# Kernel optimization log

Measured on AMD Instinct MI355X. Metric: run time of the kernel, lower is better.

Reference implementation:

```python
import jax, jax.numpy as jnp
import numpy as np

N = 8192
TEMP = 0.5
EPS = 1e-12


def _normalize(z):
    # F.normalize(z, p=2, dim=1): x / max(||x||, eps)
    n = jnp.sqrt(jnp.sum(z * z, axis=1, keepdims=True))
    return z / jnp.maximum(n, EPS)


def _gcn(edge_index, edge_weight, x, w, b):
    # torch.sparse.mm(adj, x @ w): out[row] += adj[row, col] * support[col]
    support = x @ w
    msg = support[edge_index[1]] * edge_weight[:, None]
    return jax.ops.segment_sum(msg, edge_index[0], num_segments=N) + b


def _encoder(edge_index, edge_weight, feat, w_l1a, b_l1a, w_l1b, b_l1b, w_g1, b_g1, w_g2, b_g2):
    x = jax.nn.relu(feat @ w_l1a + b_l1a) @ w_l1b + b_l1b  # [N, 32]
    h = jax.nn.relu(_gcn(edge_index, edge_weight, x, w_g1, b_g1))  # [N, hid]
    return _gcn(edge_index, edge_weight, h, w_g2, b_g2)  # [N, act_fn]


def _proj(h, w_fc1, b_fc1, w_fc2, b_fc2):
    return jax.nn.elu(h @ w_fc1 + b_fc1) @ w_fc2 + b_fc2


def _loss(z1, z2):
    z1n = _normalize(z1)
    z2n = _normalize(z2)
    refl = jnp.exp((z1n @ z1n.T) / TEMP)      # [N, N]
    between = jnp.exp((z1n @ z2n.T) / TEMP)   # [N, N]
    denom = refl.sum(1) + between.sum(1) - jnp.diagonal(refl)
    return -jnp.log(jnp.diagonal(between) / denom)


def setup_inputs() -> dict:
    key = jax.random.key(0)
    ks = jax.random.split(key, 20)
    E = 262144
    in_dim, hid_dim, act_fn, out_dim = 512, 256, 128, 64

    def kaiming(k, shape):
        fan_in = shape[0]
        bound = np.sqrt(6.0 / fan_in)
        return jax.random.uniform(k, shape, jnp.float32, -bound, bound)

    return {
        "feat1": jax.random.normal(ks[0], (N, in_dim), jnp.float32),
        "feat2": jax.random.normal(ks[1], (N, in_dim), jnp.float32),
        "edge_index1": jax.random.randint(ks[2], (2, E), 0, N, jnp.int32),
        "edge_weight1": jax.random.uniform(ks[3], (E,), jnp.float32),
        "edge_index2": jax.random.randint(ks[4], (2, E), 0, N, jnp.int32),
        "edge_weight2": jax.random.uniform(ks[5], (E,), jnp.float32),
        "w_l1a": kaiming(ks[6], (in_dim, 64)),
        "b_l1a": jnp.zeros((64,), jnp.float32),
        "w_l1b": kaiming(ks[7], (64, 32)),
        "b_l1b": jnp.zeros((32,), jnp.float32),
        "w_g1": kaiming(ks[8], (32, hid_dim)),
        "b_g1": jnp.zeros((hid_dim,), jnp.float32),
        "w_g2": kaiming(ks[9], (hid_dim, act_fn)),
        "b_g2": jnp.zeros((act_fn,), jnp.float32),
        "w_fc1": kaiming(ks[10], (act_fn, out_dim)),
        "b_fc1": jnp.zeros((out_dim,), jnp.float32),
        "w_fc2": kaiming(ks[11], (out_dim, act_fn)),
        "b_fc2": jnp.zeros((act_fn,), jnp.float32),
    }


def reference(feat1, feat2, edge_index1, edge_weight1, edge_index2, edge_weight2,
              w_l1a, b_l1a, w_l1b, b_l1b, w_g1, b_g1, w_g2, b_g2,
              w_fc1, b_fc1, w_fc2, b_fc2):
    h1 = _encoder(edge_index1, edge_weight1, feat1, w_l1a, b_l1a, w_l1b, b_l1b, w_g1, b_g1, w_g2, b_g2)
    h2 = _encoder(edge_index2, edge_weight2, feat2, w_l1a, b_l1a, w_l1b, b_l1b, w_g1, b_g1, w_g2, b_g2)
    z1 = _proj(h1, w_fc1, b_fc1, w_fc2, b_fc2)
    z2 = _proj(h2, w_fc1, b_fc1, w_fc2, b_fc2)
    l1 = _loss(z1, z2)
    l2 = _loss(z2, z1)
    return ((l1 + l2) * 0.5).mean()
```

## Files before the change

kernel.cpp:

```cpp
#include <hip/hip_runtime.h>
#include <hip/hip_bf16.h>
#include <math.h>


#define NROWS 8192
#define MROWS 16384
#define NEDGE 262144
#define ECAP 128

typedef __attribute__((ext_vector_type(8))) short bf16x8;
typedef __attribute__((ext_vector_type(4))) float f32x4;
typedef __attribute__((ext_vector_type(2))) float f32x2;
typedef __attribute__((ext_vector_type(8))) int i32x8;
typedef long long i64;

__device__ __forceinline__ short f2bf(float f){
  union { float f; unsigned u; } cv; cv.f = f;
  unsigned u = cv.u;
  unsigned r = (u + 0x7fffu + ((u >> 16) & 1u)) >> 16;
  return (short)r;
}
__device__ __forceinline__ f32x4 mfma16(bf16x8 a, bf16x8 b, f32x4 c){
  return __builtin_amdgcn_mfma_f32_16x16x32_bf16(a, b, c, 0, 0, 0);
}
__device__ __forceinline__ float fexp2(float x){
#if __has_builtin(__builtin_amdgcn_exp2f)
  return __builtin_amdgcn_exp2f(x);
#else
  return exp2f(x);
#endif
}

template<int CTRL>
__device__ __forceinline__ float dpp_add(float v){
  int s = __builtin_amdgcn_update_dpp(0, __builtin_bit_cast(int, v),
                                      CTRL, 0xf, 0xf, true);
  return v + __builtin_bit_cast(float, s);
}
__device__ __forceinline__ float red16(float v){
  v = dpp_add<0x101>(v);
  v = dpp_add<0x102>(v);
  v = dpp_add<0x104>(v);
  v = dpp_add<0x108>(v);
  return v;
}

__device__ unsigned char f2e4m3_sw(float f){
  float a = fabsf(f);
  unsigned s = (__float_as_uint(f)>>24)&0x80u;
  if (!(a>0.f)) return (unsigned char)s;
  if (a>448.f) a=448.f;
  int e; frexpf(a,&e);
  int eff=e-1;
  unsigned code;
  if (eff<-6){
    float q=rintf(a*512.f);
    code=(unsigned)q; if(code>7)code=7;
  } else {
    float q=rintf(a*exp2f((float)(3-eff)));
    unsigned mant=(unsigned)q;
    if(mant>=16){mant=8;eff++;}
    if(eff>8) return (unsigned char)(s|0x7e);
    code=((unsigned)(eff+7)<<3)|(mant-8);
  }
  return (unsigned char)(s|code);
}
__device__ __forceinline__ unsigned short pack2fp8(float a, float b){
#if __has_builtin(__builtin_amdgcn_cvt_pk_fp8_f32)
  int v = __builtin_amdgcn_cvt_pk_fp8_f32(a, b, 0, false);
  return (unsigned short)(v & 0xffff);
#else
  return (unsigned short)((unsigned)f2e4m3_sw(a) | ((unsigned)f2e4m3_sw(b)<<8));
#endif
}

struct WtArgs {
  const float* src[6];
  short* dst[6];
  int K[6], N[6];
  int off[7];
  int nwt;
};
__global__ void setup_k(WtArgs a){
  int i = blockIdx.x*256 + threadIdx.x;
  if (i >= a.off[6]) return;
  int s = 0;
  #pragma unroll
  for (int j=1;j<6;j++) if (i >= a.off[j]) s=j;
  int l = i - a.off[s];
  int K=a.K[s], N=a.N[s];
  int k=l/N, n=l-k*N;
  a.dst[s][(long)n*K+k] = f2bf(a.src[s][l]);
}

__global__ __launch_bounds__(256) void fm2_k(const float* __restrict__ F0, const float* __restrict__ F1,
    const short* __restrict__ Wa, const float* __restrict__ ba,
    const short* __restrict__ Wb, const float* __restrict__ bb, short* __restrict__ xb,
    const int* __restrict__ ei1, const float* __restrict__ w1, int* __restrict__ deg1,
    int2* __restrict__ eg1,
    const int* __restrict__ ei2, const float* __restrict__ w2, int* __restrict__ deg2,
    int2* __restrict__ eg2){
  __shared__ short As[32*520];
  __shared__ short a1s[32*72];
  const int tid = threadIdx.x;
  if (blockIdx.x < 2*(NEDGE/256)){
    int b = blockIdx.x;
    bool g2 = (b >= NEDGE/256);
    const int* ei = g2 ? ei2 : ei1;
    const float* w = g2 ? w2 : w1;
    int* deg = g2 ? deg2 : deg1;
    int2* eg = g2 ? eg2 : eg1;
    int e = (b % (NEDGE/256))*256 + tid;
    int r = ei[e];
    int c = ei[NEDGE + e];
    float wv = w[e];
    int p = atomicAdd(&deg[r], 1);
    eg[(long)r*ECAP + p] = make_int2(c, __float_as_int(wv));
    return;
  }
  const int m0 = (blockIdx.x - 2*(NEDGE/256))*32;
  const float* F = (m0 < NROWS) ? (F0 + (long)m0*512) : (F1 + (long)(m0-NROWS)*512);
  {
    float4 st[16];
    #pragma unroll
    for (int i=0;i<16;i++) st[i] = *(const float4*)(F + (long)(i*256+tid)*4);
    #pragma unroll
    for (int i=0;i<16;i++){
      int idx = i*256+tid, row = idx>>7, c4 = idx&127;
      unsigned lo = (unsigned)(unsigned short)f2bf(st[i].x) | ((unsigned)(unsigned short)f2bf(st[i].y)<<16);
      unsigned hi = (unsigned)(unsigned short)f2bf(st[i].z) | ((unsigned)(unsigned short)f2bf(st[i].w)<<16);
      uint2 o = {lo, hi};
      *(uint2*)&As[row*520 + c4*4] = o;
    }
  }
  __syncthreads();
  const int wave = tid>>6, lane = tid&63, quad = lane>>4, cl = lane&15;
  f32x4 zero = {0.f,0.f,0.f,0.f};
  {
    const int wno = wave*16;
    f32x4 acc[2] = {zero, zero};
    #pragma unroll
    for (int kc=0;kc<16;kc++){
      const int ko = kc*32 + quad*8;
      bf16x8 a0 = *(const bf16x8*)&As[(cl)*520 + ko];
      bf16x8 a1 = *(const bf16x8*)&As[(16+cl)*520 + ko];
      bf16x8 b = *(const bf16x8*)(Wa + (long)(wno + cl)*512 + ko);
      acc[0] = mfma16(a0, b, acc[0]);
      acc[1] = mfma16(a1, b, acc[1]);
    }
    int col = wno + cl;
    float bv = ba[col];
    #pragma unroll
    for (int mt=0;mt<2;mt++)
      #pragma unroll
      for (int r=0;r<4;r++)
        a1s[(mt*16 + quad*4 + r)*72 + col] = f2bf(fmaxf(acc[mt][r] + bv, 0.f));
  }
  __syncthreads();
  if (wave < 2){
    f32x4 acc2[2] = {zero, zero};
    #pragma unroll
    for (int kc=0;kc<2;kc++){
      const int ko = kc*32 + quad*8;
      bf16x8 a = *(const bf16x8*)&a1s[(wave*16+cl)*72 + ko];
      #pragma unroll
      for (int nt=0;nt<2;nt++){
        bf16x8 b = *(const bf16x8*)(Wb + (long)(nt*16 + cl)*64 + ko);
        acc2[nt] = mfma16(a, b, acc2[nt]);
      }
    }
    #pragma unroll
    for (int nt=0;nt<2;nt++){
      int col = nt*16 + cl;
      float bv = bb[col];
      #pragma unroll
      for (int r=0;r<4;r++)
        xb[(long)(m0 + wave*16 + quad*4 + r)*32 + col] = f2bf(acc2[nt][r] + bv);
    }
  }
}

__device__ __forceinline__ void acc8(float* acc, int4 v, float f){
  const unsigned* u = (const unsigned*)&v;
  #pragma unroll
  for (int i=0;i<4;i++){
    union{unsigned x; float y;} lo, hi;
    lo.x = u[i] << 16;
    hi.x = u[i] & 0xffff0000u;
    acc[2*i]   = fmaf(f, lo.y, acc[2*i]);
    acc[2*i+1] = fmaf(f, hi.y, acc[2*i+1]);
  }
}
template<int C>
__device__ __forceinline__ void gather_row(float* acc, const short* sb,
                                           const int2* eg, int s, int e){
  int k = s;
  for (; k+16 <= e; k+=16){
    int2 cw[16]; int4 v[16];
    #pragma unroll
    for (int u=0;u<16;u++) cw[u] = eg[k+u];
    #pragma unroll
    for (int u=0;u<16;u++) v[u] = *(const int4*)(sb + (long)cw[u].x*C);
    #pragma unroll
    for (int u=0;u<16;u++) acc8(acc, v[u], __int_as_float(cw[u].y));
  }
  for (; k+4 <= e; k+=4){
    int2 c0=eg[k], c1=eg[k+1], c2=eg[k+2], c3=eg[k+3];
    int4 v0 = *(const int4*)(sb + (long)c0.x*C);
    int4 v1 = *(const int4*)(sb + (long)c1.x*C);
    int4 v2 = *(const int4*)(sb + (long)c2.x*C);
    int4 v3 = *(const int4*)(sb + (long)c3.x*C);
    acc8(acc,v0,__int_as_float(c0.y)); acc8(acc,v1,__int_as_float(c1.y));
    acc8(acc,v2,__int_as_float(c2.y)); acc8(acc,v3,__int_as_float(c3.y));
  }
  for (; k < e; k++){
    int2 c0 = eg[k];
    int4 v0 = *(const int4*)(sb + (long)c0.x*C);
    acc8(acc,v0,__int_as_float(c0.y));
  }
}

__global__ __launch_bounds__(256) void gg_k(const short* __restrict__ xb,
    const int* __restrict__ deg1, const int2* __restrict__ eg1,
    const int* __restrict__ deg2, const int2* __restrict__ eg2,
    const short* __restrict__ Wg1, const float* __restrict__ bg1,
    const short* __restrict__ Wg2, short* __restrict__ s2){
  __shared__ short axs[16*40];
  __shared__ short hbs[16*264];
  __shared__ float tmp[16][4][3][8];
  const int tid = threadIdx.x;
  const int m0 = blockIdx.x*16;
  {
    const int g = tid & 3, h = (tid>>2)&3, sub = tid >> 4;
    const int row = m0 + sub;
    const int* deg; const int2* eg; int soff, lr;
    if (row < NROWS){ deg=deg1; eg=eg1; soff=0; lr=row; }
    else            { deg=deg2; eg=eg2; soff=NROWS; lr=row-NROWS; }
    const short* sb = xb + (long)soff*32 + g*8;
    int d = deg[lr];
    int st = (d*h)>>2, en = (d*(h+1))>>2;
    float acc[8];
    #pragma unroll
    for (int j=0;j<8;j++) acc[j] = 0.f;
    gather_row<32>(acc, sb, eg + (long)lr*ECAP, st, en);
    if (h > 0){
      #pragma unroll
      for (int j=0;j<8;j++) tmp[sub][g][h-1][j] = acc[j];
    }
    __syncthreads();
    if (h == 0){
      #pragma unroll
      for (int j=0;j<8;j++)
        acc[j] = ((acc[j] + tmp[sub][g][0][j]) + tmp[sub][g][1][j]) + tmp[sub][g][2][j];
      int4 ov;
      unsigned* ou = (unsigned*)&ov;
      #pragma unroll
      for (int i=0;i<4;i++)
        ou[i] = (unsigned)(unsigned short)f2bf(acc[2*i]) | ((unsigned)(unsigned short)f2bf(acc[2*i+1])<<16);
      *(int4*)&axs[sub*40 + g*8] = ov;
    }
  }
  __syncthreads();
  const int wave = tid>>6, lane = tid&63, quad = lane>>4, cl = lane&15;
  f32x4 zero = {0.f,0.f,0.f,0.f};
  {
    const int wno = wave*64;
    f32x4 acc[4];
    #pragma unroll
    for (int i=0;i<4;i++) acc[i]=zero;
    const int ko = quad*8;
    bf16x8 a0 = *(const bf16x8*)&axs[cl*40 + ko];
    bf16x8 b[4];
    #pragma unroll
    for (int nt=0;nt<4;nt++)
      b[nt] = *(const bf16x8*)(Wg1 + (long)(wno + nt*16 + cl)*32 + ko);
    #pragma unroll
    for (int nt=0;nt<4;nt++)
      acc[nt] = mfma16(a0, b[nt], acc[nt]);
    #pragma unroll
    for (int nt=0;nt<4;nt++){
      int col = wno + nt*16 + cl;
      float bv = bg1[col];
      #pragma unroll
      for (int r=0;r<4;r++)
        hbs[(quad*4 + r)*264 + col] = f2bf(fmaxf(acc[nt][r] + bv, 0.f));
    }
  }
  __syncthreads();
  {
    const int wno = wave*32;
    f32x4 acc[2] = {zero, zero};
    #pragma unroll
    for (int kc=0;kc<8;kc++){
      const int ko = kc*32 + quad*8;
      bf16x8 a = *(const bf16x8*)&hbs[cl*264 + ko];
      #pragma unroll
      for (int nt=0;nt<2;nt++){
        bf16x8 b = *(const bf16x8*)(Wg2 + (long)(wno + nt*16 + cl)*256 + ko);
        acc[nt] = mfma16(a, b, acc[nt]);
      }
    }
    #pragma unroll
    for (int nt=0;nt<2;nt++){
      int col = wno + nt*16 + cl;
      #pragma unroll
      for (int r=0;r<4;r++)
        s2[(long)(m0 + quad*4 + r)*128 + col] = f2bf(acc[nt][r]);
    }
  }
}

__global__ __launch_bounds__(256) void pn_k(const short* __restrict__ s2,
    const int* __restrict__ deg1, const int2* __restrict__ eg1,
    const int* __restrict__ deg2, const int2* __restrict__ eg2,
    const float* __restrict__ bg2,
    const short* __restrict__ Wf1, const float* __restrict__ bf1,
    const short* __restrict__ Wf2, const float* __restrict__ bf2,
    unsigned short* __restrict__ Zf, float* __restrict__ bdot){
  __shared__ short hs[32*136];
  __shared__ short t2s[32*72];
  __shared__ float zs[32*132];
  __shared__ float sp[8][32];
  __shared__ float dp[8][16];
  __shared__ float rnS[32];
  const float SQKE = 1.6986436f;
  const int tid = threadIdx.x;
  const int wave = tid>>6, lane = tid&63, quad = lane>>4, cl = lane&15;
  const int m0h = blockIdx.x*16;
  {
    const int g = tid & 15, sub = tid >> 4;
    #pragma unroll 1
    for (int pass=0; pass<2; pass++){
      int hrow = pass*16 + sub;
      int lr = m0h + (hrow & 15);
      const int* deg; const int2* eg; long soff;
      if (hrow < 16){ deg=deg1; eg=eg1; soff=0; }
      else          { deg=deg2; eg=eg2; soff=NROWS; }
      const short* sb = s2 + soff*128 + g*8;
      float acc[8];
      #pragma unroll
      for (int j=0;j<8;j++) acc[j] = bg2[g*8+j];
      gather_row<128>(acc, sb, eg + (long)lr*ECAP, 0, deg[lr]);
      int4 ov;
      unsigned* ou = (unsigned*)&ov;
      #pragma unroll
      for (int i=0;i<4;i++)
        ou[i] = (unsigned)(unsigned short)f2bf(acc[2*i]) | ((unsigned)(unsigned short)f2bf(acc[2*i+1])<<16);
      *(int4*)&hs[hrow*136 + g*8] = ov;
    }
  }
  __syncthreads();
  f32x4 zero = {0.f,0.f,0.f,0.f};
  {
    const int wno = wave*16;
    f32x4 acc[2] = {zero, zero};
    #pragma unroll
    for (int kc=0;kc<4;kc++){
      const int ko = kc*32 + quad*8;
      bf16x8 a[2], b;
      #pragma unroll
      for (int mt=0;mt<2;mt++)
        a[mt] = *(const bf16x8*)&hs[(mt*16+cl)*136 + ko];
      b = *(const bf16x8*)(Wf1 + (long)(wno + cl)*128 + ko);
      #pragma unroll
      for (int mt=0;mt<2;mt++) acc[mt] = mfma16(a[mt], b, acc[mt]);
    }
    int col = wno + cl;
    float bv = bf1[col];
    #pragma unroll
    for (int mt=0;mt<2;mt++)
      #pragma unroll
      for (int r=0;r<4;r++){
        float v = acc[mt][r] + bv;
        v = (v > 0.f) ? v : expm1f(v);
        t2s[(mt*16 + quad*4 + r)*72 + col] = f2bf(v);
      }
  }
  __syncthreads();
  {
    const int wno = wave*32;
    f32x4 acc[2][2];
    #pragma unroll
    for (int i=0;i<2;i++){ acc[i][0]=zero; acc[i][1]=zero; }
    #pragma unroll
    for (int kc=0;kc<2;kc++){
      const int ko = kc*32 + quad*8;
      bf16x8 a[2], b[2];
      #pragma unroll
      for (int mt=0;mt<2;mt++)
        a[mt] = *(const bf16x8*)&t2s[(mt*16+cl)*72 + ko];
      #pragma unroll
      for (int nt=0;nt<2;nt++)
        b[nt] = *(const bf16x8*)(Wf2 + (long)(wno + nt*16 + cl)*64 + ko);
      #pragma unroll
      for (int mt=0;mt<2;mt++)
        #pragma unroll
        for (int nt=0;nt<2;nt++)
          acc[mt][nt] = mfma16(a[mt], b[nt], acc[mt][nt]);
    }
    #pragma unroll
    for (int mt=0;mt<2;mt++)
      #pragma unroll
      for (int nt=0;nt<2;nt++){
        int col = wno + nt*16 + cl;
        float bv = bf2[col];
        #pragma unroll
        for (int r=0;r<4;r++)
          zs[(mt*16 + quad*4 + r)*132 + col] = acc[mt][nt][r] + bv;
      }
  }
  __syncthreads();
  {
    int row = tid & 31, qtr = tid >> 5;
    const float* zr = &zs[row*132 + qtr*16];
    float s = 0.f;
    #pragma unroll 8
    for (int c=0;c<16;c++) s += zr[c]*zr[c];
    sp[qtr][row] = s;
    if (row < 16){
      const float* zb_ = &zs[(row+16)*132 + qtr*16];
      float d = 0.f;
      #pragma unroll 8
      for (int c=0;c<16;c++) d += zr[c]*zb_[c];
      dp[qtr][row] = d;
    }
  }
  __syncthreads();
  if (tid < 32){
    float ssq = ((sp[0][tid]+sp[1][tid])+(sp[2][tid]+sp[3][tid]))
              + ((sp[4][tid]+sp[5][tid])+(sp[6][tid]+sp[7][tid]));
    rnS[tid] = 1.f / fmaxf(sqrtf(ssq), 1e-12f);
  }
  __syncthreads();
  if (tid < 16){
    float dot = ((dp[0][tid]+dp[1][tid])+(dp[2][tid]+dp[3][tid]))
              + ((dp[4][tid]+dp[5][tid])+(dp[6][tid]+dp[7][tid]));
    bdot[m0h + tid] = dot * rnS[tid] * rnS[tid+16];
  }
  {
    int lr = tid >> 3;
    int grow = (lr < 16) ? (m0h + lr) : (NROWS + m0h + lr - 16);
    float s = rnS[lr] * SQKE;
    int p0 = (tid & 7)*8;
    long gbase = (long)(grow>>4)*1024 + (long)(p0>>4)*256
               + (long)(grow&15)*16 + (p0&15);
    #pragma unroll
    for (int pp=0;pp<8;pp++){
      int p = p0 + pp;
      Zf[gbase + pp] = pack2fp8(zs[lr*132 + 2*p]*s, zs[lr*132 + 2*p + 1]*s);
    }
  }
}

__global__ __launch_bounds__(256,4) void gram3_k(const unsigned char* __restrict__ Zf,
                                                 float* __restrict__ P){
  __shared__ float srow[4][64];
  __shared__ float scol[4][64];
  const int wave = threadIdx.x>>6, lane = threadIdx.x&63;
  const int t = blockIdx.x*4 + wave;
  int ti = (int)((513.0f - sqrtf(513.0f*513.0f - 8.0f*(float)t))*0.5f);
  while ((ti+1)*256 - ((ti+1)*ti)/2 <= t) ti++;
  while (ti*256 - (ti*(ti-1))/2 > t) ti--;
  const int tj = ti + (t - (ti*256 - (ti*(ti-1))/2));
  const unsigned char* za = Zf + (long)ti*8192 + lane*32;
  const unsigned char* zb = Zf + (long)tj*8192 + lane*32;
  const int quad = lane>>4, cl = lane&15;

  f32x4 zero = {0.f,0.f,0.f,0.f};
  f32x2 z2 = {0.f,0.f};
  f32x2 cs[4] = {z2,z2,z2,z2};

  i32x8 Bf[4];
  #pragma unroll
  for (int nt=0;nt<4;nt++)
    Bf[nt] = *(const i32x8*)(zb + nt*2048);

  i32x8 Ab[2];
  Ab[0] = *(const i32x8*)(za);
  Ab[1] = *(const i32x8*)(za + 2048);

  auto exprow = [&](const f32x4* ar, int mt){
    f32x2 r01 = z2, r23 = z2;
    #pragma unroll
    for (int nt=0;nt<4;nt++){
      f32x4 v = ar[nt];
      float e0 = fexp2(v[0]), e1 = fexp2(v[1]);
      float e2 = fexp2(v[2]), e3 = fexp2(v[3]);
      f32x2 p01 = {e0,e1}, p23 = {e2,e3};
      r01 += p01; r23 += p23;
      cs[nt] += p01; cs[nt] += p23;
    }
    float s0 = red16(r01.x);
    float s1 = red16(r01.y);
    float s2 = red16(r23.x);
    float s3 = red16(r23.y);
    if (cl==0){
      f32x4 rv = {s0, s1, s2, s3};
      *(f32x4*)&srow[wave][mt*16 + quad*4] = rv;
    }
  };

  const int SC1 = 0x7F;
  f32x4 acc2[2][4];
  #pragma unroll
  for (int nt=0;nt<4;nt++)
    acc2[0][nt] = __builtin_amdgcn_mfma_scale_f32_16x16x128_f8f6f4(
        Ab[0], Bf[nt], zero, 0, 0, 0, SC1, 0, SC1);
  #pragma unroll
  for (int mt=1; mt<4; mt++){
    const int cur = mt&1, prv = cur^1;
    if (mt<3)
      Ab[prv] = *(const i32x8*)(za + (mt+1)*2048);
    #pragma unroll
    for (int nt=0;nt<4;nt++)
      acc2[cur][nt] = __builtin_amdgcn_mfma_scale_f32_16x16x128_f8f6f4(
          Ab[cur], Bf[nt], zero, 0, 0, 0, SC1, 0, SC1);
    exprow(&acc2[prv][0], mt-1);
  }
  exprow(&acc2[1][0], 3);

  __threadfence_block();
  P[((long)ti*256 + tj)*64 + lane] = srow[wave][lane];
  if (ti != tj){
    #pragma unroll
    for (int nt=0;nt<4;nt++){
      float s = cs[nt].x + cs[nt].y;
      s += __shfl_xor(s,16); s += __shfl_xor(s,32);
      if (quad==0) scol[wave][nt*16 + cl] = s;
    }
    __threadfence_block();
    P[((long)tj*256 + ti)*64 + lane] = scol[wave][lane];
  }
}

__global__ __launch_bounds__(256) void rloss_k(const float* __restrict__ P,
                                               const float* __restrict__ bdot,
                                               float* __restrict__ out){
  __shared__ float ps[8][32][2];
  const float E2 = 7.3890560989306495f;
  int t = threadIdx.x;
  int rloc = t & 31, grp = t >> 5;
  int i = blockIdx.x*32 + rloc;
  int j = i + NROWS;
  const float* p1 = P + (long)(i>>6)*256*64 + (long)grp*32*64 + (i&63);
  const float* p2 = P + (long)(j>>6)*256*64 + (long)grp*32*64 + (j&63);
  float s1 = 0.f, s2 = 0.f;
  #pragma unroll 8
  for (int b=0;b<32;b++){ s1 += p1[b*64]; s2 += p2[b*64]; }
  ps[grp][rloc][0] = s1;
  ps[grp][rloc][1] = s2;
  __syncthreads();
  if (t < 64){
    float term = 0.f;
    if (t < 32){
      float a1 = 0.f, a2 = 0.f;
      #pragma unroll
      for (int g=0; g<8; g++){ a1 += ps[g][t][0]; a2 += ps[g][t][1]; }
      int ii = blockIdx.x*32 + t;
      float lb = 2.f * bdot[ii];
      term = 0.5f * ((logf(a1 - E2) - lb) + (logf(a2 - E2) - lb));
    }
    #pragma unroll
    for (int m=1; m<64; m<<=1) term += __shfl_xor(term, m);
    if (t==0) atomicAdd(out, term / (float)NROWS);
  }
}

extern "C" void kernel_launch(void* const* d_in, const int* in_sizes, int n_in,
                              void* d_out, int out_size, void* d_ws, size_t ws_size,
                              hipStream_t stream){
  const float* feat1 = (const float*)d_in[0];
  const float* feat2 = (const float*)d_in[1];
  const int*   ei1   = (const int*)d_in[2];
  const float* w1    = (const float*)d_in[3];
  const int*   ei2   = (const int*)d_in[4];
  const float* w2    = (const float*)d_in[5];
  const float* w_l1a = (const float*)d_in[6];
  const float* b_l1a = (const float*)d_in[7];
  const float* w_l1b = (const float*)d_in[8];
  const float* b_l1b = (const float*)d_in[9];
  const float* w_g1  = (const float*)d_in[10];
  const float* b_g1  = (const float*)d_in[11];
  const float* w_g2  = (const float*)d_in[12];
  const float* b_g2  = (const float*)d_in[13];
  const float* w_fc1 = (const float*)d_in[14];
  const float* b_fc1 = (const float*)d_in[15];
  const float* w_fc2 = (const float*)d_in[16];
  const float* b_fc2 = (const float*)d_in[17];

  float* P = (float*)d_ws;
  char* base = (char*)d_ws;
  size_t off = (size_t)17<<20;
  auto alloc = [&](size_t bytes)->void*{
    void* r = base + off;
    off = (off + bytes + 255) & ~(size_t)255;
    return r;
  };
  short* xb   = (short*)alloc((size_t)MROWS*32*2);
  short* s2   = (short*)alloc((size_t)MROWS*128*2);
  short* wl1a_t = (short*)alloc(512*64*2);
  short* wl1b_t = (short*)alloc(64*32*2);
  short* wg1_t  = (short*)alloc(32*256*2);
  short* wg2_t  = (short*)alloc(256*128*2);
  short* wfc1_t = (short*)alloc(128*64*2);
  short* wfc2_t = (short*)alloc(64*128*2);
  unsigned short* Zf = (unsigned short*)alloc((size_t)MROWS*128);
  int*   deg1 = (int*)alloc(NROWS*4);
  int*   deg2 = (int*)alloc(NROWS*4);
  int2*  eg1 = (int2*)alloc((size_t)NROWS*ECAP*8);
  int2*  eg2 = (int2*)alloc((size_t)NROWS*ECAP*8);
  float* bdot  = (float*)alloc(NROWS*4);

  hipMemsetAsync(deg1, 0, (size_t)2*NROWS*4, stream);
  hipMemsetAsync(d_out, 0, sizeof(float), stream);

  WtArgs wa;
  wa.src[0]=w_l1a; wa.dst[0]=wl1a_t; wa.K[0]=512; wa.N[0]=64;
  wa.src[1]=w_l1b; wa.dst[1]=wl1b_t; wa.K[1]=64;  wa.N[1]=32;
  wa.src[2]=w_g1;  wa.dst[2]=wg1_t;  wa.K[2]=32;  wa.N[2]=256;
  wa.src[3]=w_g2;  wa.dst[3]=wg2_t;  wa.K[3]=256; wa.N[3]=128;
  wa.src[4]=w_fc1; wa.dst[4]=wfc1_t; wa.K[4]=128; wa.N[4]=64;
  wa.src[5]=w_fc2; wa.dst[5]=wfc2_t; wa.K[5]=64;  wa.N[5]=128;
  wa.off[0]=0;
  for (int i=0;i<6;i++) wa.off[i+1] = wa.off[i] + wa.K[i]*wa.N[i];
  wa.nwt = (wa.off[6]+255)/256;

  setup_k<<<wa.nwt,256,0,stream>>>(wa);
  fm2_k<<<2*(NEDGE/256) + MROWS/32,256,0,stream>>>(feat1, feat2, wl1a_t, b_l1a,
      wl1b_t, b_l1b, xb,
      ei1, w1, deg1, eg1,
      ei2, w2, deg2, eg2);
  gg_k<<<MROWS/16,256,0,stream>>>(xb, deg1,eg1, deg2,eg2,
                                  wg1_t, b_g1, wg2_t, s2);
  pn_k<<<NROWS/16,256,0,stream>>>(s2, deg1,eg1, deg2,eg2, b_g2,
                                  wfc1_t, b_fc1, wfc2_t, b_fc2, Zf, bdot);
  gram3_k<<<8224,256,0,stream>>>((const unsigned char*)Zf, P);
  rloss_k<<<NROWS/32,256,0,stream>>>(P, bdot, (float*)d_out);
}
```

Before: 219.0 us.

## Partition edge bucketing by row residue per XCD with persistent work-claiming blocks

Edge bucketing now runs in 1024 persistent blocks that claim 256-edge chunks through global atomic counters. Each block reads the XCC ID and handles only edges whose destination row falls in its residue class (row & 7), so degree atomics and bucket writes for a row come from one XCD and stay local to its L2. A second pass over all residues picks up any leftover work. The cost is that every block scans every chunk of edge rows, so row-index reads rise about eightfold, and each chunk claim adds two barriers and a counter atomic.

```diff
diff --git a/kernel.cpp b/kernel.cpp
--- a/kernel.cpp
+++ b/kernel.cpp
@@ -7,6 +7,8 @@
 #define MROWS 16384
 #define NEDGE 262144
 #define ECAP 128
+#define NCHUNK (NEDGE/256)
+#define NFB 1024
 
 typedef __attribute__((ext_vector_type(8))) short bf16x8;
 typedef __attribute__((ext_vector_type(4))) float f32x4;
@@ -99,26 +101,48 @@
     const int* __restrict__ ei1, const float* __restrict__ w1, int* __restrict__ deg1,
     int2* __restrict__ eg1,
     const int* __restrict__ ei2, const float* __restrict__ w2, int* __restrict__ deg2,
-    int2* __restrict__ eg2){
+    int2* __restrict__ eg2,
+    int* __restrict__ ctrs){
   __shared__ short As[32*520];
   __shared__ short a1s[32*72];
+  __shared__ int claim;
   const int tid = threadIdx.x;
-  if (blockIdx.x < 2*(NEDGE/256)){
-    int b = blockIdx.x;
-    bool g2 = (b >= NEDGE/256);
-    const int* ei = g2 ? ei2 : ei1;
-    const float* w = g2 ? w2 : w1;
-    int* deg = g2 ? deg2 : deg1;
-    int2* eg = g2 ? eg2 : eg1;
-    int e = (b % (NEDGE/256))*256 + tid;
-    int r = ei[e];
-    int c = ei[NEDGE + e];
-    float wv = w[e];
-    int p = atomicAdd(&deg[r], 1);
-    eg[(long)r*ECAP + p] = make_int2(c, __float_as_int(wv));
+  if (blockIdx.x < NFB){
+    int xcd = 0;
+    asm volatile("s_getreg_b32 %0, hwreg(HW_REG_XCC_ID)" : "=s"(xcd));
+    xcd &= 7;
+    #pragma unroll 1
+    for (int pass = 0; pass < 2; ++pass){
+      int nidx = (pass == 0) ? 2 : 16;
+      #pragma unroll 1
+      for (int i0 = 0; i0 < nidx; ++i0){
+        int idx = (pass == 0) ? (i0*8 + xcd) : i0;
+        const bool g2 = (idx >= 8);
+        const int res = idx & 7;
+        const int* ei = g2 ? ei2 : ei1;
+        const float* w = g2 ? w2 : w1;
+        int* deg = g2 ? deg2 : deg1;
+        int2* eg = g2 ? eg2 : eg1;
+        while (true){
+          if (tid == 0) claim = atomicAdd(&ctrs[idx], 1);
+          __syncthreads();
+          int c = claim;
+          __syncthreads();
+          if (c >= NCHUNK) break;
+          int e = c*256 + tid;
+          int r = ei[e];
+          if ((r & 7) == res){
+            int col = ei[NEDGE + e];
+            float wv = w[e];
+            int p = atomicAdd(&deg[r], 1);
+            eg[(long)r*ECAP + p] = make_int2(col, __float_as_int(wv));
+          }
+        }
+      }
+    }
     return;
   }
-  const int m0 = (blockIdx.x - 2*(NEDGE/256))*32;
+  const int m0 = (blockIdx.x - NFB)*32;
   const float* F = (m0 < NROWS) ? (F0 + (long)m0*512) : (F1 + (long)(m0-NROWS)*512);
   {
     float4 st[16];
@@ -607,11 +631,12 @@
   unsigned short* Zf = (unsigned short*)alloc((size_t)MROWS*128);
   int*   deg1 = (int*)alloc(NROWS*4);
   int*   deg2 = (int*)alloc(NROWS*4);
+  int*   ctrs = (int*)alloc(16*4);
   int2*  eg1 = (int2*)alloc((size_t)NROWS*ECAP*8);
   int2*  eg2 = (int2*)alloc((size_t)NROWS*ECAP*8);
   float* bdot  = (float*)alloc(NROWS*4);
 
-  hipMemsetAsync(deg1, 0, (size_t)2*NROWS*4, stream);
+  hipMemsetAsync(deg1, 0, (size_t)2*NROWS*4 + 256, stream);
   hipMemsetAsync(d_out, 0, sizeof(float), stream);
 
   WtArgs wa;
@@ -626,10 +651,10 @@
   wa.nwt = (wa.off[6]+255)/256;
 
   setup_k<<<wa.nwt,256,0,stream>>>(wa);
-  fm2_k<<<2*(NEDGE/256) + MROWS/32,256,0,stream>>>(feat1, feat2, wl1a_t, b_l1a,
+  fm2_k<<<NFB + MROWS/32,256,0,stream>>>(feat1, feat2, wl1a_t, b_l1a,
       wl1b_t, b_l1b, xb,
       ei1, w1, deg1, eg1,
-      ei2, w2, deg2, eg2);
+      ei2, w2, deg2, eg2, ctrs);
   gg_k<<<MROWS/16,256,0,stream>>>(xb, deg1,eg1, deg2,eg2,
                                   wg1_t, b_g1, wg2_t, s2);
   pn_k<<<NROWS/16,256,0,stream>>>(s2, deg1,eg1, deg2,eg2, b_g2,
```

Measured after the change: 597.8 us. +172.9%, slower.
